# Optimization experiments

Measured on AMD Instinct MI355X. Metric: run time of the kernel, lower is better.

The kernel has to match this reference:

```python
import jax, jax.numpy as jnp
import numpy as np

T, D, TR, CC, L = 4096, 512, 64, 64, 3  # time, input_size, trace, context, num_blocks


def setup_inputs() -> dict:
    key = jax.random.key(0)
    ks = jax.random.split(key, 10)
    x = jax.random.normal(ks[0], (T, D), dtype=jnp.float32)
    state = jnp.zeros((L, 1, TR, CC), dtype=jnp.float32)  # initial recurrent state (real part; imag is 0)
    start = jax.random.uniform(ks[1], (T,)) < 0.02  # episode-reset mask
    Wtr = jax.random.normal(ks[2], (L, TR, D), dtype=jnp.float32) / np.float32(np.sqrt(D))
    Wc = jax.random.normal(ks[3], (L, TR, D), dtype=jnp.float32) / np.float32(np.sqrt(D))
    a = jax.random.uniform(ks[4], (L, TR), minval=1e-6, maxval=0.1)
    b = 2 * jnp.pi / jnp.exp(jax.random.uniform(ks[5], (L, CC), minval=0.0, maxval=float(np.log(10000.0))))
    F = 2 * TR * CC
    W0 = jax.random.normal(ks[6], (L, D, F), dtype=jnp.float32) * np.float32(0.01 / np.sqrt(F))  # default_init scale=0.01
    b0 = jnp.zeros((L, D)); g0 = jnp.ones((L, D)); beta0 = jnp.zeros((L, D))
    W1 = jax.random.normal(ks[7], (L, D, D), dtype=jnp.float32) / np.float32(np.sqrt(D))
    b1 = jnp.zeros((L, D)); g1 = jnp.ones((L, D)); beta1 = jnp.zeros((L, D))
    return dict(x=x, state=state, start=start, Wtr=Wtr, Wc=Wc, a=a, b=b,
                W0=W0, b0=b0, g0=g0, beta0=beta0, W1=W1, b1=b1, g1=g1, beta1=beta1)


def _layernorm(z, g, b):
    m = jnp.mean(z, axis=-1, keepdims=True)
    v = jnp.mean((z - m) ** 2, axis=-1, keepdims=True)
    return (z - m) / jnp.sqrt(v + 1e-5) * g + b


def _sffm(x, st0, start, Wtr, Wc, a, b, W0, b0, g0, bb0, W1, b1, g1, bb1):
    t_len = x.shape[0]
    tr = x @ Wtr.T           # [T, TR]
    ct = x @ Wc.T            # [T, CC] (context proj also has trace_size outputs)
    pre = jnp.abs(tr[:, :, None] * ct[:, None, :])            # [T, TR, CC]
    pre = pre / (1e-8 + jnp.sum(pre, axis=(-2, -1), keepdims=True))
    # complex decay per (trace, context) pair: exp((-|a| + i b) * dt)
    ab = (-jnp.abs(a))[:, None] + 1j * b[None, :]             # [TR, CC] complex64

    def combine(carry, inc):
        ps, s, i = carry
        st, xx, j = inc
        s = s * jnp.logical_not(st)                            # reset gating
        dt = (j - i).astype(jnp.float32)[:, None, None]
        new = s * jnp.exp(ab[None] * dt) + xx
        return (jnp.logical_or(st, ps), new, j)

    ts = jnp.arange(t_len + 1, dtype=jnp.int32)
    sb = jnp.concatenate([jnp.zeros((1, 1, 1), bool), start.reshape(t_len, 1, 1)], axis=0)
    xs = jnp.concatenate([st0.astype(jnp.complex64), pre.astype(jnp.complex64)], axis=0)
    _, ns, _ = jax.lax.associative_scan(combine, (sb, xs, ts), axis=0)
    ns = ns[1:]                                                # [T, TR, CC] complex

    s = ns.reshape(t_len, TR * CC)
    mag = jnp.log1p(jnp.abs(s))
    ang = jnp.angle(s)
    scaled = jnp.concatenate([mag * jnp.sin(ang), mag * jnp.cos(ang)], axis=-1)  # [T, 2*TR*CC]
    z = jax.nn.leaky_relu(_layernorm(scaled @ W0.T + b0, g0, bb0))
    z = jax.nn.leaky_relu(_layernorm(z @ W1.T + b1, g1, bb1))
    return z


def reference(x, state, start, Wtr, Wc, a, b, W0, b0, g0, beta0, W1, b1, g1, beta1):
    z = x
    for l in range(L):
        z = _sffm(x, state[l], start, Wtr[l], Wc[l], a[l], b[l],
                  W0[l], b0[l], g0[l], beta0[l], W1[l], b1[l], g1[l], beta1[l])
        x = x + z
    return z  # NSFFM returns the last block's y
```

## Files before the change

kernel.cpp:

```cpp
#include <hip/hip_runtime.h>
#include <hip/hip_bf16.h>
#include <math.h>

#define T_LEN 4096
#define D_DIM 512
#define F_DIM 8192
#define NCHUNK 64
#define CLEN 64

typedef short short8 __attribute__((ext_vector_type(8)));
typedef float f32x4 __attribute__((ext_vector_type(4)));
typedef unsigned short u16;
typedef unsigned int u32;

__device__ inline float wave_sum(float v) {
#pragma unroll
  for (int o = 32; o; o >>= 1) v += __shfl_xor(v, o);
  return v;
}

__device__ inline u16 f2bf_bits(float v) {
  __hip_bfloat16 h = __float2bfloat16(v);
  return *(u16*)&h;
}

__device__ inline void gl_lds16(const void* g, void* l) {
  __builtin_amdgcn_global_load_lds((const __attribute__((address_space(1))) void*)g,
                                   (__attribute__((address_space(3))) void*)l, 16, 0, 0);
}

__global__ void detect_start(const unsigned char* __restrict__ s8, int* __restrict__ mode) {
  __shared__ int found;
  if (threadIdx.x == 0) found = 0;
  __syncthreads();
  for (int i = threadIdx.x; i < 4096; i += 256)
    if ((i & 3) && s8[i]) found = 1;
  __syncthreads();
  if (threadIdx.x == 0) mode[0] = found;
}

__device__ inline int read_start(const unsigned char* s8, const int* s32, int mode, int t) {
  return mode ? (int)s8[t] : s32[t];
}

__global__ void f2bf(const float* __restrict__ s, u16* __restrict__ d, int n) {
  int i = blockIdx.x * 256 + threadIdx.x;
  if (i < n) d[i] = f2bf_bits(s[i]);
}

__global__ void k_w0perm(const float* __restrict__ src, u16* __restrict__ dst) {
  int i = blockIdx.x * 256 + threadIdx.x;
  int d = i >> 13, f = i & 8191;
  int r = f >> 7, rem = f & 127;
  int c = rem >> 1, b = rem & 1;
  dst[i] = f2bf_bits(src[(size_t)d * 8192 + b * 4096 + r * 64 + c]);
}

__global__ void k_wcat(const float* __restrict__ wtr, const float* __restrict__ wc,
                       u16* __restrict__ dst) {
  int i = blockIdx.x * 256 + threadIdx.x;
  float v = (i < 64 * D_DIM) ? wtr[i] : wc[i - 64 * D_DIM];
  dst[i] = f2bf_bits(v);
}

template <int BM, int BN, int WR, int WC>
__global__ __launch_bounds__(256) void gemm_bt(const u16* __restrict__ A,
                                               const u16* __restrict__ B,
                                               float* __restrict__ C, int M, int N, int K) {
  constexpr int BK = 32;
  constexpr int MT = BM / (WR * 16);
  constexpr int NT = BN / (WC * 16);
  constexpr int AG = BM / 64;
  constexpr int BG = BN / 64;
  __shared__ u16 sA[BM * BK];
  __shared__ u16 sB[BN * BK];
  const int m0 = blockIdx.x * BM;
  const int n0 = blockIdx.y * BN;
  const int tid = threadIdx.x;
  const int wave = tid >> 6;
  const int lane = tid & 63;
  const int wr = wave / WC;
  const int wc = wave % WC;
  const int row_l = tid >> 2;
  const int c8 = (tid & 3) << 3;
  const int frow = lane & 15;
  const int fcol = (lane >> 4) << 3;

  f32x4 acc[MT][NT];
#pragma unroll
  for (int i = 0; i < MT; ++i)
#pragma unroll
    for (int j = 0; j < NT; ++j) acc[i][j] = (f32x4){0.f, 0.f, 0.f, 0.f};

  for (int k0 = 0; k0 < K; k0 += BK) {
#pragma unroll
    for (int j = 0; j < AG; ++j) {
      uint4 v = *(const uint4*)(A + (size_t)(m0 + j * 64 + row_l) * K + (k0 + c8));
      *(uint4*)(sA + (j * 64 + row_l) * BK + c8) = v;
    }
#pragma unroll
    for (int j = 0; j < BG; ++j) {
      uint4 v = *(const uint4*)(B + (size_t)(n0 + j * 64 + row_l) * K + (k0 + c8));
      *(uint4*)(sB + (j * 64 + row_l) * BK + c8) = v;
    }
    __syncthreads();
    short8 af[MT], bfr[NT];
#pragma unroll
    for (int i = 0; i < MT; ++i)
      af[i] = *(const short8*)(sA + (wr * MT * 16 + i * 16 + frow) * BK + fcol);
#pragma unroll
    for (int j = 0; j < NT; ++j)
      bfr[j] = *(const short8*)(sB + (wc * NT * 16 + j * 16 + frow) * BK + fcol);
#pragma unroll
    for (int i = 0; i < MT; ++i)
#pragma unroll
      for (int j = 0; j < NT; ++j)
        acc[i][j] = __builtin_amdgcn_mfma_f32_16x16x32_bf16(af[i], bfr[j], acc[i][j], 0, 0, 0);
    __syncthreads();
  }
#pragma unroll
  for (int i = 0; i < MT; ++i) {
    const int rbase = m0 + wr * MT * 16 + i * 16 + ((lane >> 4) << 2);
#pragma unroll
    for (int j = 0; j < NT; ++j) {
      const int col = n0 + wc * NT * 16 + j * 16 + (lane & 15);
#pragma unroll
      for (int rg = 0; rg < 4; ++rg) C[(size_t)(rbase + rg) * N + col] = acc[i][j][rg];
    }
  }
}

__global__ __launch_bounds__(256) void gemm128(const u16* __restrict__ A,
                                               const u16* __restrict__ B,
                                               float* __restrict__ Cp, size_t pstride, int N,
                                               int Ktot) {
  __shared__ u16 sA[128 * 32];
  __shared__ u16 sB[128 * 32];
  const int tid = threadIdx.x;
  const int wave = tid >> 6;
  const int lane = tid & 63;
  const int wr = wave >> 1;
  const int wc = wave & 1;
  const int m0 = blockIdx.x * 128;
  const int n0 = blockIdx.y * 128;
  const int ks = blockIdx.z;
  const int Kper = Ktot / gridDim.z;
  const int kb = ks * Kper;
  const int row_l = tid >> 2;
  const int c8 = (tid & 3) << 3;
  const int frow = lane & 15;
  const int fcol = (lane >> 4) << 3;

  f32x4 acc[4][4];
#pragma unroll
  for (int i = 0; i < 4; ++i)
#pragma unroll
    for (int j = 0; j < 4; ++j) acc[i][j] = (f32x4){0.f, 0.f, 0.f, 0.f};

  for (int k0 = kb; k0 < kb + Kper; k0 += 32) {
#pragma unroll
    for (int j = 0; j < 2; ++j) {
      gl_lds16(A + (size_t)(m0 + j * 64 + row_l) * Ktot + (k0 + c8), sA + j * 2048 + wave * 512);
      gl_lds16(B + (size_t)(n0 + j * 64 + row_l) * Ktot + (k0 + c8), sB + j * 2048 + wave * 512);
    }
    asm volatile("s_waitcnt vmcnt(0)" ::: "memory");
    __syncthreads();
    short8 af[4], bfr[4];
#pragma unroll
    for (int i = 0; i < 4; ++i)
      af[i] = *(const short8*)(sA + (wr * 64 + i * 16 + frow) * 32 + fcol);
#pragma unroll
    for (int j = 0; j < 4; ++j)
      bfr[j] = *(const short8*)(sB + (wc * 64 + j * 16 + frow) * 32 + fcol);
#pragma unroll
    for (int i = 0; i < 4; ++i)
#pragma unroll
      for (int j = 0; j < 4; ++j)
        acc[i][j] = __builtin_amdgcn_mfma_f32_16x16x32_bf16(af[i], bfr[j], acc[i][j], 0, 0, 0);
    __syncthreads();
  }
#pragma unroll
  for (int i = 0; i < 4; ++i) {
    const int rbase = m0 + wr * 64 + i * 16 + ((lane >> 4) << 2);
#pragma unroll
    for (int j = 0; j < 4; ++j) {
      const int col = n0 + wc * 64 + j * 16 + (lane & 15);
#pragma unroll
      for (int rg = 0; rg < 4; ++rg)
        Cp[(size_t)ks * pstride + (size_t)(rbase + rg) * N + col] = acc[i][j][rg];
    }
  }
}

__global__ void prep_pq(const float* __restrict__ trct, float* __restrict__ p,
                        float* __restrict__ pT, float* __restrict__ q) {
  int t = blockIdx.x;
  int lane = threadIdx.x;
  float tr = trct[t * 128 + lane];
  float ct = trct[t * 128 + 64 + lane];
  float ap = fabsf(tr), aq = fabsf(ct);
  float Sp = wave_sum(ap);
  float Sq = wave_sum(aq);
  float denom = 1e-8f + Sp * Sq;
  p[t * 64 + lane] = ap;
  pT[lane * T_LEN + t] = ap;
  q[t * 64 + lane] = aq / denom;
}

__global__ void scan_phase1(const float* __restrict__ pT, const float* __restrict__ q,
                            const unsigned char* __restrict__ st8, const int* __restrict__ st32,
                            const int* __restrict__ modep, const float* __restrict__ a,
                            const float* __restrict__ b, float4* __restrict__ chunkbuf) {
  int chunk = blockIdx.x, r = blockIdx.y, c = threadIdx.x;
  int mode = modep[0];
  int t0 = chunk * CLEN;
  float rho = expf(-fabsf(a[r]));
  float bb = b[c];
  float er = rho * cosf(bb), ei = rho * sinf(bb);
  float pv = pT[r * T_LEN + t0 + c];
  int sv = read_start(st8, st32, mode, t0 + c);
  float Ar = 1.f, Ai = 0.f, Br = 0.f, Bi = 0.f;
  const float* qrow = q + (size_t)t0 * 64 + c;
#pragma unroll 8
  for (int i = 0; i < CLEN; ++i) {
    float qt = qrow[i * 64];
    float pt = __shfl(pv, i);
    int st = __shfl(sv, i);
    float pre = pt * qt;
    float cer = st ? 0.f : er;
    float cei = st ? 0.f : ei;
    float nAr = cer * Ar - cei * Ai;
    Ai = cer * Ai + cei * Ar;
    Ar = nAr;
    float nBr = cer * Br - cei * Bi + pre;
    Bi = cer * Bi + cei * Br;
    Br = nBr;
  }
  chunkbuf[((size_t)chunk * 64 + r) * 64 + c] = make_float4(Ar, Ai, Br, Bi);
}

__global__ void scan_phase2(const float4* __restrict__ chunkbuf, const float* __restrict__ state,
                            float2* __restrict__ s0buf) {
  int r = blockIdx.x, c = threadIdx.x;
  float Sr = state[r * 64 + c], Si = 0.f;
  for (int k = 0; k < NCHUNK; ++k) {
    s0buf[((size_t)k * 64 + r) * 64 + c] = make_float2(Sr, Si);
    float4 ab = chunkbuf[((size_t)k * 64 + r) * 64 + c];
    float nSr = ab.x * Sr - ab.y * Si + ab.z;
    Si = ab.x * Si + ab.y * Sr + ab.w;
    Sr = nSr;
  }
}

__global__ void scan_phase3(const float* __restrict__ pT, const float* __restrict__ q,
                            const unsigned char* __restrict__ st8, const int* __restrict__ st32,
                            const int* __restrict__ modep, const float* __restrict__ a,
                            const float* __restrict__ b, const float2* __restrict__ s0buf,
                            u32* __restrict__ scaled, int c0) {
  int chunk = c0 + blockIdx.x, r = blockIdx.y, c = threadIdx.x;
  int mode = modep[0];
  int t0 = chunk * CLEN;
  float rho = expf(-fabsf(a[r]));
  float bb = b[c];
  float er = rho * cosf(bb), ei = rho * sinf(bb);
  float pv = pT[r * T_LEN + t0 + c];
  int sv = read_start(st8, st32, mode, t0 + c);
  float2 s0 = s0buf[((size_t)chunk * 64 + r) * 64 + c];
  float Sr = s0.x, Si = s0.y;
  int tl0 = (chunk - c0) * CLEN;
  const float* qrow = q + (size_t)t0 * 64 + c;
  u32* drow = scaled + (size_t)tl0 * 4096 + r * 64 + c;
#pragma unroll 4
  for (int i = 0; i < CLEN; ++i) {
    float qt = qrow[i * 64];
    float pt = __shfl(pv, i);
    int st = __shfl(sv, i);
    float pre = pt * qt;
    float cer = st ? 0.f : er;
    float cei = st ? 0.f : ei;
    float nSr = cer * Sr - cei * Si + pre;
    Si = cer * Si + cei * Sr;
    Sr = nSr;
    float m2 = fmaf(Sr, Sr, Si * Si);
    float rsq = rsqrtf(fmaxf(m2, 1e-30f));
    float m = m2 * rsq;
    float sc = __log2f(1.0f + m) * 0.6931471805599453f * rsq;
    u32 pack = ((u32)f2bf_bits(sc * Sr) << 16) | (u32)f2bf_bits(sc * Si);
    drow[(size_t)i * 4096] = pack;
  }
}

__global__ void ln_act(const float* __restrict__ parts, int KS, size_t pstride,
                       const float* __restrict__ bias, const float* __restrict__ gam,
                       const float* __restrict__ bet, u16* __restrict__ zbf,
                       const float* __restrict__ xsrc, float* __restrict__ xdst,
                       u16* __restrict__ xbf_next, float* __restrict__ finout) {
  __shared__ float red[8];
  int t = blockIdx.x, tid = threadIdx.x;
  size_t o = (size_t)t * D_DIM + tid;
  float v0 = bias[tid];
  float v1 = bias[tid + 256];
  for (int ks = 0; ks < KS; ++ks) {
    v0 += parts[(size_t)ks * pstride + o];
    v1 += parts[(size_t)ks * pstride + o + 256];
  }
  float s = wave_sum(v0 + v1);
  if ((tid & 63) == 0) red[tid >> 6] = s;
  __syncthreads();
  float mean = (red[0] + red[1] + red[2] + red[3]) * (1.f / 512.f);
  float d0 = v0 - mean, d1 = v1 - mean;
  float s2 = wave_sum(d0 * d0 + d1 * d1);
  if ((tid & 63) == 0) red[4 + (tid >> 6)] = s2;
  __syncthreads();
  float var = (red[4] + red[5] + red[6] + red[7]) * (1.f / 512.f);
  float rstd = rsqrtf(var + 1e-5f);
  float z0 = d0 * rstd * gam[tid] + bet[tid];
  float z1 = d1 * rstd * gam[tid + 256] + bet[tid + 256];
  z0 = z0 > 0.f ? z0 : 0.01f * z0;
  z1 = z1 > 0.f ? z1 : 0.01f * z1;
  if (zbf) { zbf[o] = f2bf_bits(z0); zbf[o + 256] = f2bf_bits(z1); }
  if (xdst) {
    float x0 = xsrc[o] + z0, x1 = xsrc[o + 256] + z1;
    xdst[o] = x0; xdst[o + 256] = x1;
    if (xbf_next) { xbf_next[o] = f2bf_bits(x0); xbf_next[o + 256] = f2bf_bits(x1); }
  }
  if (finout) { finout[o] = z0; finout[o + 256] = z1; }
}

__global__ void err_signal(float* __restrict__ out, float code) {
  if (threadIdx.x == 0) out[0] = code;
}

extern "C" void kernel_launch(void* const* d_in, const int* in_sizes, int n_in, void* d_out,
                              int out_size, void* d_ws, size_t ws_size, hipStream_t stream) {
  const float* x_in = (const float*)d_in[0];
  const float* state = (const float*)d_in[1];
  const unsigned char* start8 = (const unsigned char*)d_in[2];
  const int* start32 = (const int*)d_in[2];
  const float* Wtr = (const float*)d_in[3];
  const float* Wc = (const float*)d_in[4];
  const float* a_in = (const float*)d_in[5];
  const float* b_in = (const float*)d_in[6];
  const float* W0 = (const float*)d_in[7];
  const float* b0 = (const float*)d_in[8];
  const float* g0 = (const float*)d_in[9];
  const float* beta0 = (const float*)d_in[10];
  const float* W1 = (const float*)d_in[11];
  const float* b1 = (const float*)d_in[12];
  const float* g1 = (const float*)d_in[13];
  const float* beta1 = (const float*)d_in[14];
  float* out = (float*)d_out;

  char* w = (char*)d_ws;
  auto alloc = [&](size_t bytes) {
    char* ptr = w;
    w += (bytes + 255) & ~(size_t)255;
    return ptr;
  };
  float* x_ws = (float*)alloc(4ull * T_LEN * D_DIM);
  u16* xbf = (u16*)alloc(2ull * T_LEN * D_DIM);
  u16* wcat = (u16*)alloc(2ull * 128 * D_DIM);
  u16* w0bf = (u16*)alloc(2ull * D_DIM * F_DIM);
  u16* w1bf = (u16*)alloc(2ull * 3 * D_DIM * D_DIM);
  float* trct = (float*)alloc(4ull * T_LEN * 128);
  float* pbuf = (float*)alloc(4ull * T_LEN * 64);
  float* pTbuf = (float*)alloc(4ull * T_LEN * 64);
  float* qbuf = (float*)alloc(4ull * T_LEN * 64);
  float4* chunkbuf = (float4*)alloc(16ull * NCHUNK * 64 * 64);
  float2* s0buf = (float2*)alloc(8ull * NCHUNK * 64 * 64);
  u16* z0bf = (u16*)alloc(2ull * T_LEN * D_DIM);
  int* modep = (int*)alloc(256);
  size_t base1 = (size_t)(w - (char*)d_ws);

  if (n_in != 15) {
    err_signal<<<1, 64, 0, stream>>>(out, 9e6f + 1000.f * n_in);
    return;
  }
  const size_t MB = 1ull << 20;
  int KS, nseg;
  if (ws_size >= base1 + 32 * MB + 64 * MB) { KS = 4; nseg = 1; }
  else if (ws_size >= base1 + 32 * MB + 32 * MB) { KS = 4; nseg = 2; }
  else if (ws_size >= base1 + 16 * MB + 32 * MB) { KS = 2; nseg = 2; }
  else if (ws_size >= base1 + 16 * MB + 16 * MB) { KS = 2; nseg = 4; }
  else if (ws_size >= base1 + 8 * MB + 16 * MB) { KS = 1; nseg = 4; }
  else {
    err_signal<<<1, 64, 0, stream>>>(out, 9e6f);
    return;
  }
  const int KSw1 = (KS >= 2) ? 2 : 1;
  const int seg_rows = T_LEN / nseg;
  const int seg_chunks = NCHUNK / nseg;
  const size_t pstride = (size_t)T_LEN * D_DIM;
  float* ypart = (float*)alloc(4ull * KS * pstride);
  u16* scaled = (u16*)alloc(2ull * seg_rows * F_DIM);

  detect_start<<<1, 256, 0, stream>>>(start8, modep);
  f2bf<<<(T_LEN * D_DIM) / 256, 256, 0, stream>>>(x_in, xbf, T_LEN * D_DIM);
  f2bf<<<(3 * D_DIM * D_DIM) / 256, 256, 0, stream>>>(W1, w1bf, 3 * D_DIM * D_DIM);

  for (int l = 0; l < 3; ++l) {
    const float* Wtr_l = Wtr + (size_t)l * 64 * D_DIM;
    const float* Wc_l = Wc + (size_t)l * 64 * D_DIM;
    const float* a_l = a_in + l * 64;
    const float* b_l = b_in + l * 64;
    const float* W0_l = W0 + (size_t)l * D_DIM * F_DIM;
    const u16* w1bf_l = w1bf + (size_t)l * D_DIM * D_DIM;
    const float* state_l = state + (size_t)l * 64 * 64;
    const float* xsrc = (l == 0) ? x_in : x_ws;

    k_wcat<<<(128 * D_DIM) / 256, 256, 0, stream>>>(Wtr_l, Wc_l, wcat);
    k_w0perm<<<(D_DIM * F_DIM) / 256, 256, 0, stream>>>(W0_l, w0bf);

    gemm_bt<64, 64, 2, 2><<<dim3(T_LEN / 64, 2), 256, 0, stream>>>(xbf, wcat, trct, T_LEN, 128,
                                                                   D_DIM);
    prep_pq<<<T_LEN, 64, 0, stream>>>(trct, pbuf, pTbuf, qbuf);
    scan_phase1<<<dim3(NCHUNK, 64), 64, 0, stream>>>(pTbuf, qbuf, start8, start32, modep, a_l,
                                                     b_l, chunkbuf);
    scan_phase2<<<64, 64, 0, stream>>>(chunkbuf, state_l, s0buf);

    for (int h = 0; h < nseg; ++h) {
      scan_phase3<<<dim3(seg_chunks, 64), 64, 0, stream>>>(pTbuf, qbuf, start8, start32, modep,
                                                           a_l, b_l, s0buf, (u32*)scaled,
                                                           h * seg_chunks);
      gemm128<<<dim3(seg_rows / 128, D_DIM / 128, KS), 256, 0, stream>>>(
          scaled, w0bf, ypart + (size_t)h * seg_rows * D_DIM, pstride, D_DIM, F_DIM);
    }
    ln_act<<<T_LEN, 256, 0, stream>>>(ypart, KS, pstride, b0 + l * D_DIM, g0 + l * D_DIM,
                                      beta0 + l * D_DIM, z0bf, nullptr, nullptr, nullptr,
                                      nullptr);
    gemm128<<<dim3(T_LEN / 128, D_DIM / 128, KSw1), 256, 0, stream>>>(z0bf, w1bf_l, ypart,
                                                                      pstride, D_DIM, D_DIM);
    ln_act<<<T_LEN, 256, 0, stream>>>(ypart, KSw1, pstride, b1 + l * D_DIM, g1 + l * D_DIM,
                                      beta1 + l * D_DIM, nullptr, (l < 2) ? xsrc : nullptr,
                                      (l < 2) ? x_ws : nullptr, (l < 2) ? xbf : nullptr,
                                      (l == 2) ? out : nullptr);
  }
}
```

Before: 554.6 us.

## Fuse weight conversions, drop unused p buffer, closed-form chunk decay, deeper split-K

Merges the Wtr/Wc and W0 bf16 conversion kernels into one launch and removes the unused row-major p buffer write from prep_pq. In scan_phase1 the per-chunk decay product is computed in closed form (exp(64·ab), or zero when any reset falls in the chunk) instead of being accumulated each step, and fast __expf/__cosf/__sinf intrinsics replace the precise ones. When the workspace is large enough, split-K goes from 4 to 8 for the W0 GEMM and from 2 to 4 for the W1 GEMM. Fast trig on large angles (64·b) can lose accuracy, and more split-K partials mean more partial-sum traffic into the layernorm.

```diff
diff --git a/kernel.cpp b/kernel.cpp
--- a/kernel.cpp
+++ b/kernel.cpp
@@ -48,19 +48,21 @@
   if (i < n) d[i] = f2bf_bits(s[i]);
 }
 
-__global__ void k_w0perm(const float* __restrict__ src, u16* __restrict__ dst) {
+__global__ void k_conv(const float* __restrict__ wtr, const float* __restrict__ wc,
+                       u16* __restrict__ wcat, const float* __restrict__ w0,
+                       u16* __restrict__ w0bf) {
   int i = blockIdx.x * 256 + threadIdx.x;
-  int d = i >> 13, f = i & 8191;
-  int r = f >> 7, rem = f & 127;
-  int c = rem >> 1, b = rem & 1;
-  dst[i] = f2bf_bits(src[(size_t)d * 8192 + b * 4096 + r * 64 + c]);
-}
-
-__global__ void k_wcat(const float* __restrict__ wtr, const float* __restrict__ wc,
-                       u16* __restrict__ dst) {
-  int i = blockIdx.x * 256 + threadIdx.x;
-  float v = (i < 64 * D_DIM) ? wtr[i] : wc[i - 64 * D_DIM];
-  dst[i] = f2bf_bits(v);
+  if (i < 128 * D_DIM) {
+    float v = (i < 64 * D_DIM) ? wtr[i] : wc[i - 64 * D_DIM];
+    wcat[i] = f2bf_bits(v);
+  }
+  int j = i - 128 * D_DIM;
+  if (j >= 0 && j < D_DIM * F_DIM) {
+    int d = j >> 13, f = j & 8191;
+    int r = f >> 7, rem = f & 127;
+    int c = rem >> 1, b = rem & 1;
+    w0bf[j] = f2bf_bits(w0[(size_t)d * 8192 + b * 4096 + r * 64 + c]);
+  }
 }
 
 template <int BM, int BN, int WR, int WC>
@@ -192,8 +194,8 @@
   }
 }
 
-__global__ void prep_pq(const float* __restrict__ trct, float* __restrict__ p,
-                        float* __restrict__ pT, float* __restrict__ q) {
+__global__ void prep_pq(const float* __restrict__ trct, float* __restrict__ pT,
+                        float* __restrict__ q) {
   int t = blockIdx.x;
   int lane = threadIdx.x;
   float tr = trct[t * 128 + lane];
@@ -202,7 +204,6 @@
   float Sp = wave_sum(ap);
   float Sq = wave_sum(aq);
   float denom = 1e-8f + Sp * Sq;
-  p[t * 64 + lane] = ap;
   pT[lane * T_LEN + t] = ap;
   q[t * 64 + lane] = aq / denom;
 }
@@ -214,12 +215,23 @@
   int chunk = blockIdx.x, r = blockIdx.y, c = threadIdx.x;
   int mode = modep[0];
   int t0 = chunk * CLEN;
-  float rho = expf(-fabsf(a[r]));
+  float na = -fabsf(a[r]);
+  float rho = __expf(na);
   float bb = b[c];
-  float er = rho * cosf(bb), ei = rho * sinf(bb);
+  float er = rho * __cosf(bb), ei = rho * __sinf(bb);
   float pv = pT[r * T_LEN + t0 + c];
   int sv = read_start(st8, st32, mode, t0 + c);
-  float Ar = 1.f, Ai = 0.f, Br = 0.f, Bi = 0.f;
+  unsigned long long anyb = __ballot(sv != 0);
+  float Ar, Ai;
+  if (anyb) {
+    Ar = 0.f; Ai = 0.f;
+  } else {
+    float mag = __expf(64.f * na);
+    float ang = 64.f * bb;
+    Ar = mag * __cosf(ang);
+    Ai = mag * __sinf(ang);
+  }
+  float Br = 0.f, Bi = 0.f;
   const float* qrow = q + (size_t)t0 * 64 + c;
 #pragma unroll 8
   for (int i = 0; i < CLEN; ++i) {
@@ -229,9 +241,6 @@
     float pre = pt * qt;
     float cer = st ? 0.f : er;
     float cei = st ? 0.f : ei;
-    float nAr = cer * Ar - cei * Ai;
-    Ai = cer * Ai + cei * Ar;
-    Ar = nAr;
     float nBr = cer * Br - cei * Bi + pre;
     Bi = cer * Bi + cei * Br;
     Br = nBr;
@@ -260,9 +269,9 @@
   int chunk = c0 + blockIdx.x, r = blockIdx.y, c = threadIdx.x;
   int mode = modep[0];
   int t0 = chunk * CLEN;
-  float rho = expf(-fabsf(a[r]));
+  float rho = __expf(-fabsf(a[r]));
   float bb = b[c];
-  float er = rho * cosf(bb), ei = rho * sinf(bb);
+  float er = rho * __cosf(bb), ei = rho * __sinf(bb);
   float pv = pT[r * T_LEN + t0 + c];
   int sv = read_start(st8, st32, mode, t0 + c);
   float2 s0 = s0buf[((size_t)chunk * 64 + r) * 64 + c];
@@ -363,7 +372,6 @@
   u16* w0bf = (u16*)alloc(2ull * D_DIM * F_DIM);
   u16* w1bf = (u16*)alloc(2ull * 3 * D_DIM * D_DIM);
   float* trct = (float*)alloc(4ull * T_LEN * 128);
-  float* pbuf = (float*)alloc(4ull * T_LEN * 64);
   float* pTbuf = (float*)alloc(4ull * T_LEN * 64);
   float* qbuf = (float*)alloc(4ull * T_LEN * 64);
   float4* chunkbuf = (float4*)alloc(16ull * NCHUNK * 64 * 64);
@@ -378,7 +386,8 @@
   }
   const size_t MB = 1ull << 20;
   int KS, nseg;
-  if (ws_size >= base1 + 32 * MB + 64 * MB) { KS = 4; nseg = 1; }
+  if (ws_size >= base1 + 64 * MB + 64 * MB) { KS = 8; nseg = 1; }
+  else if (ws_size >= base1 + 32 * MB + 64 * MB) { KS = 4; nseg = 1; }
   else if (ws_size >= base1 + 32 * MB + 32 * MB) { KS = 4; nseg = 2; }
   else if (ws_size >= base1 + 16 * MB + 32 * MB) { KS = 2; nseg = 2; }
   else if (ws_size >= base1 + 16 * MB + 16 * MB) { KS = 2; nseg = 4; }
@@ -387,7 +396,7 @@
     err_signal<<<1, 64, 0, stream>>>(out, 9e6f);
     return;
   }
-  const int KSw1 = (KS >= 2) ? 2 : 1;
+  const int KSw1 = (KS >= 8) ? 4 : ((KS >= 2) ? 2 : 1);
   const int seg_rows = T_LEN / nseg;
   const int seg_chunks = NCHUNK / nseg;
   const size_t pstride = (size_t)T_LEN * D_DIM;
@@ -408,12 +417,11 @@
     const float* state_l = state + (size_t)l * 64 * 64;
     const float* xsrc = (l == 0) ? x_in : x_ws;
 
-    k_wcat<<<(128 * D_DIM) / 256, 256, 0, stream>>>(Wtr_l, Wc_l, wcat);
-    k_w0perm<<<(D_DIM * F_DIM) / 256, 256, 0, stream>>>(W0_l, w0bf);
-
+    k_conv<<<(128 * D_DIM + D_DIM * F_DIM) / 256, 256, 0, stream>>>(Wtr_l, Wc_l, wcat, W0_l,
+                                                                    w0bf);
     gemm_bt<64, 64, 2, 2><<<dim3(T_LEN / 64, 2), 256, 0, stream>>>(xbf, wcat, trct, T_LEN, 128,
                                                                    D_DIM);
-    prep_pq<<<T_LEN, 64, 0, stream>>>(trct, pbuf, pTbuf, qbuf);
+    prep_pq<<<T_LEN, 64, 0, stream>>>(trct, pTbuf, qbuf);
     scan_phase1<<<dim3(NCHUNK, 64), 64, 0, stream>>>(pTbuf, qbuf, start8, start32, modep, a_l,
                                                      b_l, chunkbuf);
     scan_phase2<<<64, 64, 0, stream>>>(chunkbuf, state_l, s0buf);
```

Result: no change. 549.6 us (-0.9%).
